# Kernel tuning notes

Hardware: AMD Instinct MI355X
Metric: run time of the kernel (lower is better)

## Reference

```python
import jax, jax.numpy as jnp
import numpy as np

N = 200000      # number of source simplices (columns of B)
M_SEG = 100000  # number of target simplices (rows of B)
NNZ = 400000    # ~2 nonzeros per column for a boundary operator
C_IN = 256
C_OUT = 256


def setup_inputs() -> dict:
    key = jax.random.key(0)
    k1, k2, k3, k4, k5 = jax.random.split(key, 5)
    x_src = jax.random.normal(k1, (N, C_IN), dtype=jnp.float32)
    W = jax.random.normal(k2, (C_IN, C_OUT), dtype=jnp.float32) / np.sqrt(C_IN)
    b_vals = jax.random.normal(k3, (NNZ,), dtype=jnp.float32)
    b_rows = jax.random.randint(k4, (NNZ,), 0, M_SEG, dtype=jnp.int32)
    b_cols = jax.random.randint(k5, (NNZ,), 0, N, dtype=jnp.int32)
    return {"x_src": x_src, "W": W, "b_vals": b_vals,
            "b_rows": b_rows, "b_cols": b_cols, "M": M_SEG}


def reference(x_src, W, b_vals, b_rows, b_cols, M):
    # Dense projection: nn.Linear(in, out, bias=False) -> x @ W
    x_proj = x_src @ W                                  # [N, C_out]
    # Sparse boundary matmul: out[r] += v * x_proj[c] for each (r, c, v) in B
    msgs = b_vals[:, None] * x_proj[b_cols]             # [nnz, C_out] gather
    out = jax.ops.segment_sum(msgs, b_rows, num_segments=M)  # [M, C_out] scatter-add
    return out
```

## Files before the change

kernel.cpp:

```cpp
#include <hip/hip_runtime.h>


typedef short bf16x8 __attribute__((ext_vector_type(8)));
typedef float f32x4  __attribute__((ext_vector_type(4)));

static __device__ __forceinline__ unsigned short f2bf(float f) {
    union { float f; unsigned u; } a; a.f = f;
    unsigned r = a.u + 0x7FFFu + ((a.u >> 16) & 1u);
    return (unsigned short)(r >> 16);
}

static __device__ __forceinline__ float bf2f(unsigned short h) {
    union { unsigned u; float f; } a; a.u = (unsigned)h << 16;
    return a.f;
}

__global__ __launch_bounds__(256) void wtrans_kernel(
    const float* __restrict__ W, unsigned short* __restrict__ Wt)
{
    int k = blockIdx.x;
    int n = threadIdx.x;
    Wt[(size_t)n * 256 + k] = f2bf(W[(size_t)k * 256 + n]);
}

__global__ __launch_bounds__(256) void hist_kernel(
    const int* __restrict__ b_rows, int* __restrict__ cnt, int nnz)
{
    int i = blockIdx.x * 256 + threadIdx.x;
    if (i < nnz) atomicAdd(&cnt[b_rows[i]], 1);
}

__global__ __launch_bounds__(1024) void scan_part_kernel(
    const int* __restrict__ cnt, int* __restrict__ partials, int M)
{
    int tid = threadIdx.x;
    int base = blockIdx.x * 4096;
    int s = 0;
    #pragma unroll
    for (int k = 0; k < 4; ++k) {
        int i = base + k * 1024 + tid;
        if (i < M) s += cnt[i];
    }
    #pragma unroll
    for (int d = 1; d < 64; d <<= 1) s += __shfl_xor(s, d);
    __shared__ int wsum[16];
    int lane = tid & 63, wid = tid >> 6;
    if (lane == 0) wsum[wid] = s;
    __syncthreads();
    if (tid == 0) {
        int t = 0;
        #pragma unroll
        for (int w = 0; w < 16; ++w) t += wsum[w];
        partials[blockIdx.x] = t;
    }
}

__global__ __launch_bounds__(64) void scan_mid_kernel(
    int* __restrict__ partials, int* __restrict__ off, int np, int M)
{
    int lane = threadIdx.x;
    int v = (lane < np) ? partials[lane] : 0;
    int x = v;
    #pragma unroll
    for (int d = 1; d < 64; d <<= 1) { int y = __shfl_up(x, d); if (lane >= d) x += y; }
    if (lane < np) partials[lane] = x - v;
    if (lane == 63) off[M] = x;
}

__global__ __launch_bounds__(1024) void scan_apply_kernel(
    const int* __restrict__ cnt, const int* __restrict__ partials,
    int* __restrict__ off, int* __restrict__ cursor, int M)
{
    int tid = threadIdx.x;
    int base = blockIdx.x * 4096 + tid * 4;
    int4 v = make_int4(0, 0, 0, 0);
    if (base + 3 < M) v = *reinterpret_cast<const int4*>(cnt + base);
    else {
        if (base + 0 < M) v.x = cnt[base + 0];
        if (base + 1 < M) v.y = cnt[base + 1];
        if (base + 2 < M) v.z = cnt[base + 2];
    }
    int s1 = v.x + v.y, s2 = s1 + v.z, tsum = s2 + v.w;
    int x = tsum;
    int lane = tid & 63, wid = tid >> 6;
    #pragma unroll
    for (int d = 1; d < 64; d <<= 1) { int y = __shfl_up(x, d); if (lane >= d) x += y; }
    __shared__ int wsum[16];
    if (lane == 63) wsum[wid] = x;
    __syncthreads();
    if (wid == 0 && lane < 16) {
        int w = wsum[lane];
        int xx = w;
        #pragma unroll
        for (int d = 1; d < 16; d <<= 1) { int y = __shfl_up(xx, d); if (lane >= d) xx += y; }
        wsum[lane] = xx - w;
    }
    __syncthreads();
    int excl = (x - tsum) + wsum[wid] + partials[blockIdx.x];
    int o0 = excl, o1 = excl + v.x, o2 = excl + s1, o3 = excl + s2;
    if (base + 0 < M) { off[base + 0] = o0; cursor[base + 0] = o0; }
    if (base + 1 < M) { off[base + 1] = o1; cursor[base + 1] = o1; }
    if (base + 2 < M) { off[base + 2] = o2; cursor[base + 2] = o2; }
    if (base + 3 < M) { off[base + 3] = o3; cursor[base + 3] = o3; }
}

__global__ __launch_bounds__(256) void fill_kernel(
    const float* __restrict__ b_vals, const int* __restrict__ b_rows,
    const int* __restrict__ b_cols, int* __restrict__ cursor,
    int* __restrict__ csr_col, float* __restrict__ csr_val, int nnz)
{
    int i = blockIdx.x * 256 + threadIdx.x;
    if (i < nnz) {
        int r = b_rows[i];
        int pos = atomicAdd(&cursor[r], 1);
        csr_col[pos] = b_cols[i];
        csr_val[pos] = b_vals[i];
    }
}

__global__ __launch_bounds__(256) void proj_kernel(
    const float* __restrict__ X, const unsigned short* __restrict__ Wt,
    unsigned short* __restrict__ xp)
{
    __shared__ __align__(16) unsigned char Ab[64 * 512];
    int tid = threadIdx.x, lane = tid & 63, wid = tid >> 6;
    int r0 = blockIdx.x * 64;

    #pragma unroll
    for (int i = 0; i < 16; ++i) {
        int row = wid * 16 + i;
        float4 f = *reinterpret_cast<const float4*>(
            X + (size_t)(r0 + row) * 256 + lane * 4);
        ushort4 h;
        h.x = f2bf(f.x); h.y = f2bf(f.y); h.z = f2bf(f.z); h.w = f2bf(f.w);
        int byte = row * 512 + ((lane * 8) ^ ((row & 7) << 4));
        *reinterpret_cast<ushort4*>(Ab + byte) = h;
    }
    __syncthreads();

    f32x4 acc[4][4] = {};
    const char* wt = reinterpret_cast<const char*>(Wt);
    int nbase = wid * 64;
    int arow = lane & 15;
    int kgrp = (lane >> 4) * 16;

    for (int s = 0; s < 8; ++s) {
        bf16x8 a[4], b[4];
        #pragma unroll
        for (int m = 0; m < 4; ++m) {
            int row = m * 16 + arow;
            int byte = row * 512 + ((s * 64 + kgrp) ^ ((row & 7) << 4));
            a[m] = *reinterpret_cast<const bf16x8*>(Ab + byte);
        }
        #pragma unroll
        for (int t = 0; t < 4; ++t) {
            int n = nbase + t * 16 + arow;
            b[t] = *reinterpret_cast<const bf16x8*>(wt + (size_t)n * 512 + s * 64 + kgrp);
        }
        #pragma unroll
        for (int m = 0; m < 4; ++m)
            #pragma unroll
            for (int t = 0; t < 4; ++t)
                acc[m][t] = __builtin_amdgcn_mfma_f32_16x16x32_bf16(a[m], b[t], acc[m][t], 0, 0, 0);
    }

    int hi = lane >> 4;
    #pragma unroll
    for (int m = 0; m < 4; ++m) {
        #pragma unroll
        for (int rr = 0; rr < 4; ++rr) {
            int row = r0 + m * 16 + hi * 4 + rr;
            ushort4 h;
            h.x = f2bf(acc[m][0][rr]);
            h.y = f2bf(acc[m][1][rr]);
            h.z = f2bf(acc[m][2][rr]);
            h.w = f2bf(acc[m][3][rr]);
            *reinterpret_cast<ushort4*>(xp + (size_t)row * 256 + wid * 64 + arow * 4) = h;
        }
    }
}

__global__ __launch_bounds__(256) void gather_kernel(
    const unsigned short* __restrict__ xp, const float* __restrict__ csr_val,
    const int* __restrict__ csr_col, const int* __restrict__ off,
    float* __restrict__ out, int M)
{
    int row = blockIdx.x * 4 + (threadIdx.x >> 6);
    if (row >= M) return;
    int lane = threadIdx.x & 63;

    int s = off[row], e = off[row + 1];
    float a0 = 0.f, a1 = 0.f, a2 = 0.f, a3 = 0.f;

    for (int j = s; j < e; j += 8) {
        int nb = e - j;
        int c[8]; float v[8]; ushort4 xs[8];
        #pragma unroll
        for (int t = 0; t < 8; ++t)
            if (t < nb) { c[t] = csr_col[j + t]; v[t] = csr_val[j + t]; }
        #pragma unroll
        for (int t = 0; t < 8; ++t)
            if (t < nb)
                xs[t] = *reinterpret_cast<const ushort4*>(
                    xp + (size_t)c[t] * 256 + lane * 4);
        #pragma unroll
        for (int t = 0; t < 8; ++t)
            if (t < nb) {
                a0 += v[t] * bf2f(xs[t].x);
                a1 += v[t] * bf2f(xs[t].y);
                a2 += v[t] * bf2f(xs[t].z);
                a3 += v[t] * bf2f(xs[t].w);
            }
    }

    int col0 = (lane >> 4) * 64 + (lane & 15);
    float* o = out + (size_t)row * 256;
    o[col0 +  0] = a0;
    o[col0 + 16] = a1;
    o[col0 + 32] = a2;
    o[col0 + 48] = a3;
}

extern "C" void kernel_launch(void* const* d_in, const int* in_sizes, int n_in,
                              void* d_out, int out_size, void* d_ws, size_t ws_size,
                              hipStream_t stream) {
    const float* x_src  = (const float*)d_in[0];
    const float* W      = (const float*)d_in[1];
    const float* b_vals = (const float*)d_in[2];
    const int*   b_rows = (const int*)d_in[3];
    const int*   b_cols = (const int*)d_in[4];

    const int C = 256;
    const int M = out_size / C;
    const int nnz = in_sizes[2];
    const int N = in_sizes[0] / C;

    char* ws = (char*)d_ws;
    unsigned short* Wt = (unsigned short*)ws;           ws += 256 * 256 * 2;
    int*   cnt     = (int*)ws;                          ws += (size_t)M * 4;
    int*   off     = (int*)ws;                          ws += (size_t)(M + 1) * 4;
    int*   cursor  = (int*)ws;                          ws += (size_t)M * 4;
    int*   partials= (int*)ws;                          ws += 64 * 4;
    int*   csr_col = (int*)ws;                          ws += (size_t)nnz * 4;
    float* csr_val = (float*)ws;                        ws += (size_t)nnz * 4;
    ws = (char*)(((size_t)ws + 63) & ~(size_t)63);
    unsigned short* xp = (unsigned short*)ws;

    float* out = (float*)d_out;

    hipMemsetAsync(cnt, 0, (size_t)M * 4, stream);

    wtrans_kernel<<<256, 256, 0, stream>>>(W, Wt);

    int nblk_nnz = (nnz + 255) / 256;
    hist_kernel<<<nblk_nnz, 256, 0, stream>>>(b_rows, cnt, nnz);

    int nb = (M + 4095) / 4096;
    scan_part_kernel<<<nb, 1024, 0, stream>>>(cnt, partials, M);
    scan_mid_kernel<<<1, 64, 0, stream>>>(partials, off, nb, M);
    scan_apply_kernel<<<nb, 1024, 0, stream>>>(cnt, partials, off, cursor, M);

    fill_kernel<<<nblk_nnz, 256, 0, stream>>>(b_vals, b_rows, b_cols, cursor,
                                              csr_col, csr_val, nnz);

    proj_kernel<<<(N + 63) / 64, 256, 0, stream>>>(x_src, Wt, xp);

    gather_kernel<<<(M + 3) / 4, 256, 0, stream>>>(xp, csr_val, csr_col, off, out, M);
}
```

Measured before the change: 220.3 us.

## Load projection A operand directly from global into registers, drop LDS staging

The projection kernel no longer stages the fp32 input rows into swizzled shared memory. Each wave now loads its A fragments straight from global memory, converts them to bf16 in registers and feeds the MFMAs. The row tile shrinks from 64 to 32 with an occupancy hint of 4 blocks per CU, removing the block barrier and LDS traffic. The trade-off is that every wave re-reads the same X rows, relying on cache to absorb the duplication. The grid assumes N is divisible by 32.

After: 312.7 us. +42.0%, slower.

```diff
diff --git a/kernel.cpp b/kernel.cpp
--- a/kernel.cpp
+++ b/kernel.cpp
@@ -13,6 +13,19 @@
 static __device__ __forceinline__ float bf2f(unsigned short h) {
     union { unsigned u; float f; } a; a.u = (unsigned)h << 16;
     return a.f;
+}
+
+static __device__ __forceinline__ unsigned pack2(float f0, float f1) {
+    return (unsigned)f2bf(f0) | ((unsigned)f2bf(f1) << 16);
+}
+
+static __device__ __forceinline__ bf16x8 cvt8(float4 lo, float4 hi) {
+    union { bf16x8 v; unsigned u[4]; } r;
+    r.u[0] = pack2(lo.x, lo.y);
+    r.u[1] = pack2(lo.z, lo.w);
+    r.u[2] = pack2(hi.x, hi.y);
+    r.u[3] = pack2(hi.z, hi.w);
+    return r.v;
 }
 
 __global__ __launch_bounds__(256) void wtrans_kernel(
@@ -118,55 +131,47 @@
     }
 }
 
-__global__ __launch_bounds__(256) void proj_kernel(
+__global__ __launch_bounds__(256, 4) void proj_kernel(
     const float* __restrict__ X, const unsigned short* __restrict__ Wt,
     unsigned short* __restrict__ xp)
 {
-    __shared__ __align__(16) unsigned char Ab[64 * 512];
-    int tid = threadIdx.x, lane = tid & 63, wid = tid >> 6;
-    int r0 = blockIdx.x * 64;
-
-    #pragma unroll
-    for (int i = 0; i < 16; ++i) {
-        int row = wid * 16 + i;
-        float4 f = *reinterpret_cast<const float4*>(
-            X + (size_t)(r0 + row) * 256 + lane * 4);
-        ushort4 h;
-        h.x = f2bf(f.x); h.y = f2bf(f.y); h.z = f2bf(f.z); h.w = f2bf(f.w);
-        int byte = row * 512 + ((lane * 8) ^ ((row & 7) << 4));
-        *reinterpret_cast<ushort4*>(Ab + byte) = h;
-    }
-    __syncthreads();
-
-    f32x4 acc[4][4] = {};
-    const char* wt = reinterpret_cast<const char*>(Wt);
-    int nbase = wid * 64;
+    int lane = threadIdx.x & 63, w = threadIdx.x >> 6;
+    int r0 = blockIdx.x * 32;
     int arow = lane & 15;
-    int kgrp = (lane >> 4) * 16;
-
+    int kg = lane >> 4;
+
+    const float* a0p = X + (size_t)(r0 + arow) * 256 + kg * 8;
+    const float* a1p = a0p + 16 * 256;
+    const char*  wt  = reinterpret_cast<const char*>(Wt);
+    int nbase = w * 64;
+    size_t boff = (size_t)(nbase + arow) * 512 + kg * 16;
+
+    f32x4 acc[2][4] = {};
+
+    #pragma unroll
     for (int s = 0; s < 8; ++s) {
-        bf16x8 a[4], b[4];
-        #pragma unroll
-        for (int m = 0; m < 4; ++m) {
-            int row = m * 16 + arow;
-            int byte = row * 512 + ((s * 64 + kgrp) ^ ((row & 7) << 4));
-            a[m] = *reinterpret_cast<const bf16x8*>(Ab + byte);
+        float4 a0l = *reinterpret_cast<const float4*>(a0p + s * 32);
+        float4 a0h = *reinterpret_cast<const float4*>(a0p + s * 32 + 4);
+        float4 a1l = *reinterpret_cast<const float4*>(a1p + s * 32);
+        float4 a1h = *reinterpret_cast<const float4*>(a1p + s * 32 + 4);
+        bf16x8 b[4];
+        #pragma unroll
+        for (int t = 0; t < 4; ++t)
+            b[t] = *reinterpret_cast<const bf16x8*>(wt + boff + (size_t)t * 16 * 512 + s * 64);
+
+        bf16x8 a0 = cvt8(a0l, a0h);
+        bf16x8 a1 = cvt8(a1l, a1h);
+
+        #pragma unroll
+        for (int t = 0; t < 4; ++t) {
+            acc[0][t] = __builtin_amdgcn_mfma_f32_16x16x32_bf16(a0, b[t], acc[0][t], 0, 0, 0);
+            acc[1][t] = __builtin_amdgcn_mfma_f32_16x16x32_bf16(a1, b[t], acc[1][t], 0, 0, 0);
         }
-        #pragma unroll
-        for (int t = 0; t < 4; ++t) {
-            int n = nbase + t * 16 + arow;
-            b[t] = *reinterpret_cast<const bf16x8*>(wt + (size_t)n * 512 + s * 64 + kgrp);
-        }
-        #pragma unroll
-        for (int m = 0; m < 4; ++m)
-            #pragma unroll
-            for (int t = 0; t < 4; ++t)
-                acc[m][t] = __builtin_amdgcn_mfma_f32_16x16x32_bf16(a[m], b[t], acc[m][t], 0, 0, 0);
     }
 
     int hi = lane >> 4;
     #pragma unroll
-    for (int m = 0; m < 4; ++m) {
+    for (int m = 0; m < 2; ++m) {
         #pragma unroll
         for (int rr = 0; rr < 4; ++rr) {
             int row = r0 + m * 16 + hi * 4 + rr;
@@ -175,7 +180,7 @@
             h.y = f2bf(acc[m][1][rr]);
             h.z = f2bf(acc[m][2][rr]);
             h.w = f2bf(acc[m][3][rr]);
-            *reinterpret_cast<ushort4*>(xp + (size_t)row * 256 + wid * 64 + arow * 4) = h;
+            *reinterpret_cast<ushort4*>(xp + (size_t)row * 256 + nbase + arow * 4) = h;
         }
     }
 }
@@ -263,7 +268,7 @@
     fill_kernel<<<nblk_nnz, 256, 0, stream>>>(b_vals, b_rows, b_cols, cursor,
                                               csr_col, csr_val, nnz);
 
-    proj_kernel<<<(N + 63) / 64, 256, 0, stream>>>(x_src, Wt, xp);
+    proj_kernel<<<N / 32, 256, 0, stream>>>(x_src, Wt, xp);
 
     gather_kernel<<<(M + 3) / 4, 256, 0, stream>>>(xp, csr_val, csr_col, off, out, M);
 }
```
